# Kernel tuning notes

Hardware: AMD Instinct MI355X
Metric: run time of the kernel (lower is better)

## Reference

```python
import jax, jax.numpy as jnp
import numpy as np

N = 100000
E = 1600000
IN_CH = 128
HEADS = 4
OUT_CH = 32
NEG_SLOPE = 0.2


def setup_inputs() -> dict:
    key = jax.random.key(0)
    k1, k2, k3, k4 = jax.random.split(key, 4)
    x = jax.random.normal(k1, (N, IN_CH), dtype=jnp.float32)
    edge_index = jax.random.randint(k2, (2, E), 0, N, dtype=jnp.int64)
    # xavier-uniform-like init scales
    w_lim = float(np.sqrt(6.0 / (IN_CH + HEADS * OUT_CH)))
    a_lim = float(np.sqrt(6.0 / (HEADS + 2 * OUT_CH)))
    weight = jax.random.uniform(k3, (IN_CH, HEADS * OUT_CH), dtype=jnp.float32, minval=-w_lim, maxval=w_lim)
    att = jax.random.uniform(k4, (1, HEADS, 2 * OUT_CH), dtype=jnp.float32, minval=-a_lim, maxval=a_lim)
    bias = jnp.zeros((HEADS * OUT_CH,), dtype=jnp.float32)
    return {"x": x, "edge_index": edge_index, "weight": weight, "att": att, "bias": bias}


def reference(x, edge_index, weight, att, bias):
    n = x.shape[0]
    h = jnp.matmul(x, weight).reshape(n, HEADS, OUT_CH)  # [N, H, C]
    src, dst = edge_index[0], edge_index[1]
    x_src = h[src]  # [E, H, C]
    x_dst = h[dst]  # [E, H, C]
    # att is [1, H, 2C]; split so we never materialize the concat tensor
    att_src = att[:, :, :OUT_CH]  # [1, H, C]
    att_dst = att[:, :, OUT_CH:]  # [1, H, C]
    alpha = (x_src * att_src).sum(-1) + (x_dst * att_dst).sum(-1)  # [E, H]
    alpha = jnp.where(alpha >= 0, alpha, NEG_SLOPE * alpha)  # leaky_relu
    # segment softmax over edges grouped by dst
    seg_max = jax.ops.segment_max(alpha, dst, num_segments=n)  # [N, H]
    alpha = jnp.exp(alpha - seg_max[dst])
    seg_sum = jax.ops.segment_sum(alpha, dst, num_segments=n)  # [N, H]
    alpha = alpha / (seg_sum[dst] + 1e-16)
    # scatter-add weighted messages
    out = jax.ops.segment_sum(alpha[:, :, None] * x_src, dst, num_segments=n)  # [N, H, C]
    out = out.reshape(n, HEADS * OUT_CH)  # concat=True
    return out + bias
```

## Files before the change

### kernel.cpp

```cpp
#include <hip/hip_runtime.h>

#define N_NODES 100000
#define N_EDGES 1600000
#define IN_CH   128
#define HEADS   4
#define OUT_CH  32
#define HID     128
#define NEG_SLOPE 0.2f

#define BNODES  1024
#define NBUCK   ((N_NODES + BNODES - 1) / BNODES)
#define NBLK    256
#define EPB     (N_EDGES / NBLK)

typedef unsigned int  uint;
typedef unsigned short ushort;

__device__ __forceinline__ ushort f2bf(float f) {
    uint u = __float_as_uint(f);
    return (ushort)((u + 0x7FFFu + ((u >> 16) & 1u)) >> 16);
}

#define BM 64
#define BK 32
__global__ __launch_bounds__(256) void k_gemm(const float* __restrict__ x,
                                              const float* __restrict__ w,
                                              ushort* __restrict__ h) {
    __shared__ float xs[BK][BM + 4];
    __shared__ float wsld[BK][HID + 4];

    const int tid  = threadIdx.x;
    const int nodeBase = blockIdx.x * BM;
    const int c0 = (tid & 15) * 8;
    const int n0 = (tid >> 4) * 4;

    float acc[4][8];
#pragma unroll
    for (int i = 0; i < 4; i++)
#pragma unroll
        for (int j = 0; j < 8; j++) acc[i][j] = 0.0f;

    for (int k0 = 0; k0 < IN_CH; k0 += BK) {
#pragma unroll
        for (int l = 0; l < 2; l++) {
            int idx  = tid + l * 256;
            int row  = idx >> 3;
            int col4 = (idx & 7) * 4;
            int n = nodeBase + row;
            float4 v = make_float4(0.f, 0.f, 0.f, 0.f);
            if (n < N_NODES) v = *reinterpret_cast<const float4*>(x + (size_t)n * IN_CH + k0 + col4);
            xs[col4 + 0][row] = v.x;
            xs[col4 + 1][row] = v.y;
            xs[col4 + 2][row] = v.z;
            xs[col4 + 3][row] = v.w;
        }
#pragma unroll
        for (int l = 0; l < 4; l++) {
            int idx  = tid + l * 256;
            int row  = idx >> 5;
            int col4 = (idx & 31) * 4;
            float4 v = *reinterpret_cast<const float4*>(w + (size_t)(k0 + row) * HID + col4);
            *reinterpret_cast<float4*>(&wsld[row][col4]) = v;
        }
        __syncthreads();

#pragma unroll
        for (int kk = 0; kk < BK; kk++) {
            float4 xv = *reinterpret_cast<const float4*>(&xs[kk][n0]);
            float4 wa = *reinterpret_cast<const float4*>(&wsld[kk][c0]);
            float4 wb = *reinterpret_cast<const float4*>(&wsld[kk][c0 + 4]);
            float xr[4] = {xv.x, xv.y, xv.z, xv.w};
            float wr[8] = {wa.x, wa.y, wa.z, wa.w, wb.x, wb.y, wb.z, wb.w};
#pragma unroll
            for (int i = 0; i < 4; i++)
#pragma unroll
                for (int j = 0; j < 8; j++)
                    acc[i][j] = fmaf(xr[i], wr[j], acc[i][j]);
        }
        __syncthreads();
    }

#pragma unroll
    for (int i = 0; i < 4; i++) {
        int n = nodeBase + n0 + i;
        if (n < N_NODES) {
            uint4 pk;
            pk.x = (uint)f2bf(acc[i][0]) | ((uint)f2bf(acc[i][1]) << 16);
            pk.y = (uint)f2bf(acc[i][2]) | ((uint)f2bf(acc[i][3]) << 16);
            pk.z = (uint)f2bf(acc[i][4]) | ((uint)f2bf(acc[i][5]) << 16);
            pk.w = (uint)f2bf(acc[i][6]) | ((uint)f2bf(acc[i][7]) << 16);
            *reinterpret_cast<uint4*>(h + (size_t)n * HID + c0) = pk;
        }
    }
}

__global__ void k_scores(const ushort* __restrict__ h, const float* __restrict__ att,
                         float* __restrict__ s_src, float* __restrict__ s_dst) {
    int i = blockIdx.x * blockDim.x + threadIdx.x;
    if (i >= N_NODES * HEADS) return;
    int head = i & (HEADS - 1);
    const uint* hp = reinterpret_cast<const uint*>(h + (size_t)i * OUT_CH);
    const float* as = att + head * (2 * OUT_CH);
    const float* ad = as + OUT_CH;
    float ss = 0.f, sd = 0.f;
#pragma unroll
    for (int q = 0; q < 4; q++) {
        uint4 u = reinterpret_cast<const uint4*>(hp)[q];
        uint uv[4] = {u.x, u.y, u.z, u.w};
#pragma unroll
        for (int t = 0; t < 4; t++) {
            int c = q * 8 + t * 2;
            float f0 = __uint_as_float(uv[t] << 16);
            float f1 = __uint_as_float(uv[t] & 0xFFFF0000u);
            ss += f0 * as[c] + f1 * as[c + 1];
            sd += f0 * ad[c] + f1 * ad[c + 1];
        }
    }
    s_src[i] = ss;
    s_dst[i] = sd;
}

__global__ __launch_bounds__(256) void k_h0(const int* __restrict__ ei,
                                            int* __restrict__ hist) {
    __shared__ int cnt[NBUCK];
    int t = threadIdx.x;
    if (t < NBUCK) cnt[t] = 0;
    __syncthreads();
    int base = blockIdx.x * EPB;
    for (int e = base + t; e < base + EPB; e += 256)
        atomicAdd(&cnt[ei[N_EDGES + e] >> 10], 1);
    __syncthreads();
    if (t < NBUCK) hist[blockIdx.x * NBUCK + t] = cnt[t];
}

__global__ __launch_bounds__(128) void k_sc0(int* __restrict__ hist,
                                             int* __restrict__ bucket_base) {
    __shared__ int sm[128];
    int t = threadIdx.x;
    int total = 0;
    if (t < NBUCK) {
#pragma unroll 8
        for (int r = 0; r < NBLK; r++) total += hist[r * NBUCK + t];
    }
    sm[t] = total;
    __syncthreads();
    for (int off = 1; off < 128; off <<= 1) {
        int v = (t >= off) ? sm[t - off] : 0;
        __syncthreads();
        sm[t] += v;
        __syncthreads();
    }
    int excl = sm[t] - total;
    if (t < NBUCK) {
        bucket_base[t] = excl;
        int running = excl;
#pragma unroll 8
        for (int r = 0; r < NBLK; r++) {
            int tmp = hist[r * NBUCK + t];
            hist[r * NBUCK + t] = running;
            running += tmp;
        }
    }
    if (t == 0) bucket_base[NBUCK] = N_EDGES;
}

__global__ __launch_bounds__(256) void k_b1(const int* __restrict__ ei,
                                            const int* __restrict__ hist,
                                            int* __restrict__ packed) {
    __shared__ int cur[NBUCK];
    int t = threadIdx.x;
    if (t < NBUCK) cur[t] = hist[blockIdx.x * NBUCK + t];
    __syncthreads();
    int base = blockIdx.x * EPB;
    for (int e = base + t; e < base + EPB; e += 256) {
        int src = ei[e], dst = ei[N_EDGES + e];
        int pos = atomicAdd(&cur[dst >> 10], 1);
        packed[pos] = (src << 10) | (dst & (BNODES - 1));
    }
}

__global__ __launch_bounds__(256) void k_b2(const int* __restrict__ packed,
                                            const int* __restrict__ bucket_base,
                                            int* __restrict__ csr_src,
                                            int* __restrict__ row_start) {
    __shared__ int cnt[BNODES];
    __shared__ int cur[BNODES];
    __shared__ int sm[256];
    int b = blockIdx.x, t = threadIdx.x;
    int beg = bucket_base[b], end = bucket_base[b + 1];
#pragma unroll
    for (int j = 0; j < 4; j++) cnt[t * 4 + j] = 0;
    __syncthreads();
    for (int e = beg + t; e < end; e += 256)
        atomicAdd(&cnt[packed[e] & (BNODES - 1)], 1);
    __syncthreads();
    int c0 = cnt[t * 4], c1 = cnt[t * 4 + 1], c2 = cnt[t * 4 + 2], c3 = cnt[t * 4 + 3];
    int tot = c0 + c1 + c2 + c3;
    sm[t] = tot;
    __syncthreads();
    for (int off = 1; off < 256; off <<= 1) {
        int v = (t >= off) ? sm[t - off] : 0;
        __syncthreads();
        sm[t] += v;
        __syncthreads();
    }
    int p0 = beg + sm[t] - tot;
    int p1 = p0 + c0, p2 = p1 + c1, p3 = p2 + c2;
    cur[t * 4] = p0; cur[t * 4 + 1] = p1; cur[t * 4 + 2] = p2; cur[t * 4 + 3] = p3;
    int nodeb = b * BNODES + t * 4;
    int pv[4] = {p0, p1, p2, p3};
#pragma unroll
    for (int j = 0; j < 4; j++)
        if (nodeb + j <= N_NODES) row_start[nodeb + j] = pv[j];
    __syncthreads();
    for (int e = beg + t; e < end; e += 256) {
        int pk = packed[e];
        int pos = atomicAdd(&cur[pk & (BNODES - 1)], 1);
        csr_src[pos] = pk >> 10;
    }
}

__global__ __launch_bounds__(64) void k_agg(const int* __restrict__ row_start,
                                            const int* __restrict__ csr_src,
                                            const float* __restrict__ s_src,
                                            const float* __restrict__ s_dst,
                                            const ushort* __restrict__ h,
                                            const float* __restrict__ bias,
                                            float* __restrict__ out) {
    int n    = blockIdx.x;
    int lane = threadIdx.x;
    int head = lane >> 4;
    float sdh = s_dst[n * HEADS + head];
    int beg = row_start[n], end = row_start[n + 1];
    const uint* hrow = reinterpret_cast<const uint*>(h);

    float acc0 = 0.f, acc1 = 0.f, sum_w = 0.f;
#pragma unroll 4
    for (int j = beg; j < end; j++) {
        int src = csr_src[j];
        float ss = s_src[src * HEADS + head];
        float a  = ss + sdh;
        a = a >= 0.f ? a : NEG_SLOPE * a;
        float wgt = __expf(a);
        sum_w += wgt;
        uint u = hrow[(size_t)src * (HID / 2) + lane];
        acc0 = fmaf(wgt, __uint_as_float(u << 16), acc0);
        acc1 = fmaf(wgt, __uint_as_float(u & 0xFFFF0000u), acc1);
    }
    float inv = 1.0f / (sum_w + 1e-16f);
    int ch = lane * 2;
    float2 bv = *reinterpret_cast<const float2*>(bias + ch);
    float2 o;
    o.x = acc0 * inv + bv.x;
    o.y = acc1 * inv + bv.y;
    *reinterpret_cast<float2*>(out + (size_t)n * HID + ch) = o;
}

extern "C" void kernel_launch(void* const* d_in, const int* in_sizes, int n_in,
                              void* d_out, int out_size, void* d_ws, size_t ws_size,
                              hipStream_t stream) {
    const float* x    = (const float*)d_in[0];
    const int*   ei   = (const int*)  d_in[1];
    const float* w    = (const float*)d_in[2];
    const float* att  = (const float*)d_in[3];
    const float* bias = (const float*)d_in[4];
    float* out = (float*)d_out;

    char* p = (char*)d_ws;
    float* s_src    = (float*)p;  p += (size_t)N_NODES * HEADS * 4;
    float* s_dst    = (float*)p;  p += (size_t)N_NODES * HEADS * 4;
    ushort* h       = (ushort*)p; p += (size_t)N_NODES * HID * 2;
    int* csr_src    = (int*)p;    p += (size_t)N_EDGES * 4;
    int* packed     = (int*)p;    p += (size_t)N_EDGES * 4;
    int* hist       = (int*)p;    p += (size_t)NBLK * NBUCK * 4;
    int* row_start  = (int*)p;    p += (size_t)(N_NODES + 1) * 4;
    int* bucket_base= (int*)p;    p += (size_t)(NBUCK + 1) * 4;

    k_gemm<<<(N_NODES + BM - 1) / BM, 256, 0, stream>>>(x, w, h);
    k_scores<<<(N_NODES * HEADS + 255) / 256, 256, 0, stream>>>(h, att, s_src, s_dst);
    k_h0<<<NBLK, 256, 0, stream>>>(ei, hist);
    k_sc0<<<1, 128, 0, stream>>>(hist, bucket_base);
    k_b1<<<NBLK, 256, 0, stream>>>(ei, hist, packed);
    k_b2<<<NBUCK, 256, 0, stream>>>(packed, bucket_base, csr_src, row_start);
    k_agg<<<N_NODES, 64, 0, stream>>>(row_start, csr_src, s_src, s_dst, h, bias, out);
}
```

Baseline: 322.7 us.

## Process four edges per wavefront with 16-byte row loads in aggregation

```diff
diff --git a/kernel.cpp b/kernel.cpp
--- a/kernel.cpp
+++ b/kernel.cpp
@@ -220,40 +220,68 @@
     }
 }
 
-__global__ __launch_bounds__(64) void k_agg(const int* __restrict__ row_start,
-                                            const int* __restrict__ csr_src,
-                                            const float* __restrict__ s_src,
-                                            const float* __restrict__ s_dst,
-                                            const ushort* __restrict__ h,
-                                            const float* __restrict__ bias,
-                                            float* __restrict__ out) {
-    int n    = blockIdx.x;
-    int lane = threadIdx.x;
-    int head = lane >> 4;
-    float sdh = s_dst[n * HEADS + head];
-    int beg = row_start[n], end = row_start[n + 1];
-    const uint* hrow = reinterpret_cast<const uint*>(h);
-
-    float acc0 = 0.f, acc1 = 0.f, sum_w = 0.f;
-#pragma unroll 4
-    for (int j = beg; j < end; j++) {
-        int src = csr_src[j];
+__global__ __launch_bounds__(256) void k_agg(const int* __restrict__ row_start,
+                                             const int* __restrict__ csr_src,
+                                             const float* __restrict__ s_src,
+                                             const float* __restrict__ s_dst,
+                                             const ushort* __restrict__ h,
+                                             const float* __restrict__ bias,
+                                             float* __restrict__ out) {
+    const int n    = blockIdx.x * 4 + (threadIdx.x >> 6);
+    const int lane = threadIdx.x & 63;
+    const int g    = lane >> 4;
+    const int q    = lane & 15;
+    const int head = q >> 2;
+
+    const float sdh = s_dst[n * HEADS + head];
+    const int beg = row_start[n], end = row_start[n + 1];
+    const uint4* __restrict__ hrow = reinterpret_cast<const uint4*>(h);
+
+    float acc[8];
+#pragma unroll
+    for (int k = 0; k < 8; k++) acc[k] = 0.f;
+    float sum_w = 0.f;
+
+#pragma unroll 2
+    for (int j = beg; j < end; j += 4) {
+        int e = j + g;
+        bool valid = e < end;
+        int src = csr_src[valid ? e : end - 1];
         float ss = s_src[src * HEADS + head];
-        float a  = ss + sdh;
-        a = a >= 0.f ? a : NEG_SLOPE * a;
-        float wgt = __expf(a);
+        uint4 u = hrow[(size_t)src * (HID / 8) + q];
+        float a = ss + sdh;
+        a = fmaxf(a, NEG_SLOPE * a);
+        float wgt = valid ? __expf(a) : 0.f;
         sum_w += wgt;
-        uint u = hrow[(size_t)src * (HID / 2) + lane];
-        acc0 = fmaf(wgt, __uint_as_float(u << 16), acc0);
-        acc1 = fmaf(wgt, __uint_as_float(u & 0xFFFF0000u), acc1);
-    }
-    float inv = 1.0f / (sum_w + 1e-16f);
-    int ch = lane * 2;
-    float2 bv = *reinterpret_cast<const float2*>(bias + ch);
-    float2 o;
-    o.x = acc0 * inv + bv.x;
-    o.y = acc1 * inv + bv.y;
-    *reinterpret_cast<float2*>(out + (size_t)n * HID + ch) = o;
+        uint uv[4] = {u.x, u.y, u.z, u.w};
+#pragma unroll
+        for (int t = 0; t < 4; t++) {
+            acc[2 * t]     = fmaf(wgt, __uint_as_float(uv[t] << 16),        acc[2 * t]);
+            acc[2 * t + 1] = fmaf(wgt, __uint_as_float(uv[t] & 0xFFFF0000u), acc[2 * t + 1]);
+        }
+    }
+
+#pragma unroll
+    for (int k = 0; k < 8; k++) {
+        acc[k] += __shfl_xor(acc[k], 16);
+        acc[k] += __shfl_xor(acc[k], 32);
+    }
+    sum_w += __shfl_xor(sum_w, 16);
+    sum_w += __shfl_xor(sum_w, 32);
+
+    if (g == 0) {
+        float inv = 1.0f / (sum_w + 1e-16f);
+        int ch = q * 8;
+        float4 b0 = *reinterpret_cast<const float4*>(bias + ch);
+        float4 b1 = *reinterpret_cast<const float4*>(bias + ch + 4);
+        float4 o0, o1;
+        o0.x = acc[0] * inv + b0.x; o0.y = acc[1] * inv + b0.y;
+        o0.z = acc[2] * inv + b0.z; o0.w = acc[3] * inv + b0.w;
+        o1.x = acc[4] * inv + b1.x; o1.y = acc[5] * inv + b1.y;
+        o1.z = acc[6] * inv + b1.z; o1.w = acc[7] * inv + b1.w;
+        *reinterpret_cast<float4*>(out + (size_t)n * HID + ch)     = o0;
+        *reinterpret_cast<float4*>(out + (size_t)n * HID + ch + 4) = o1;
+    }
 }
 
 extern "C" void kernel_launch(void* const* d_in, const int* in_sizes, int n_in,
@@ -282,5 +310,5 @@
     k_sc0<<<1, 128, 0, stream>>>(hist, bucket_base);
     k_b1<<<NBLK, 256, 0, stream>>>(ei, hist, packed);
     k_b2<<<NBUCK, 256, 0, stream>>>(packed, bucket_base, csr_src, row_start);
-    k_agg<<<N_NODES, 64, 0, stream>>>(row_start, csr_src, s_src, s_dst, h, bias, out);
-}
+    k_agg<<<N_NODES / 4, 256, 0, stream>>>(row_start, csr_src, s_src, s_dst, h, bias, out);
+}
```

Measured after the change: 319.4 us. No clear change (-1.0%).
